# Kernel optimization log

Measured on AMD Instinct MI355X. Metric: run time of the kernel, lower is better.

Reference implementation:

```python
import jax, jax.numpy as jnp
import numpy as np

N = 32768; NS = 16; C_MAIN = 128; C_MOD = 128; C_IN = 16; SHARE = 8
EPS = 1e-5; CHUNK = 1024
C_OUT = C_MAIN + C_MOD  # out_main = in_main + in_mod
C_W = C_IN // SHARE     # attention-weight channels = 2


def _bn(x, g, b, m, v):
    # BatchNorm1d in eval mode, per last-dim channel
    return (x - m) / jnp.sqrt(v + EPS) * g + b


def _knn(p, k):
    # exact kNN (self included, distance 0), chunked to bound memory
    def f(q):  # q: (CHUNK, 3)
        d = jnp.sum((q[:, None, :] - p[None, :, :]) ** 2, axis=-1)  # (CHUNK, N)
        return jax.lax.top_k(-d, k)[1]
    return jax.lax.map(f, p.reshape(-1, CHUNK, 3)).reshape(-1, k)


def setup_inputs() -> dict:
    key = jax.random.key(0)
    ks = iter(jax.random.split(key, 24))
    rn = lambda shape, s=0.1: jax.random.normal(next(ks), shape, jnp.float32) * s
    inp = {}
    inp["x_main"] = jax.random.normal(next(ks), (N, C_MAIN), jnp.float32)
    inp["x_mod"] = jax.random.normal(next(ks), (N, C_MOD), jnp.float32)
    inp["xyz"] = jax.random.uniform(next(ks), (N, 3), dtype=jnp.float32)
    inp["W_ein"] = rn((C_OUT, C_IN)); inp["b_ein"] = rn((C_IN,))
    inp["W_eout"] = rn((C_IN, C_OUT)); inp["b_eout"] = rn((C_OUT,))
    inp["Wq"] = rn((C_IN, C_IN)); inp["bq"] = rn((C_IN,))
    inp["Wk"] = rn((C_IN, C_IN)); inp["bk"] = rn((C_IN,))
    inp["Wv"] = rn((C_IN, C_IN)); inp["bv"] = rn((C_IN,))
    inp["Wp1"] = rn((3, 3)); inp["bp1"] = rn((3,))
    inp["Wp2"] = rn((3, C_IN)); inp["bp2"] = rn((C_IN,))
    inp["Wl1"] = rn((C_IN, C_W)); inp["bl1"] = rn((C_W,))
    inp["Wl2"] = rn((C_W, C_W)); inp["bl2"] = rn((C_W,))
    for name, c in (("bn_p", 3), ("bn_w1", C_IN), ("bn_w2", C_W)):
        inp[name + "_g"] = jnp.ones(c, jnp.float32)
        inp[name + "_b"] = jnp.zeros(c, jnp.float32)
        inp[name + "_m"] = jnp.zeros(c, jnp.float32)
        inp[name + "_v"] = jnp.ones(c, jnp.float32)
    return inp


def _forward(x_main, x_mod, xyz, W_ein, b_ein, W_eout, b_eout, Wq, bq, Wk, bk, Wv, bv,
             Wp1, bp1, Wp2, bp2, Wl1, bl1, Wl2, bl2,
             bn_p_g, bn_p_b, bn_p_m, bn_p_v,
             bn_w1_g, bn_w1_b, bn_w1_m, bn_w1_v,
             bn_w2_g, bn_w2_b, bn_w2_m, bn_w2_v, idx):
    x_fused = jnp.concatenate([x_main, x_mod], axis=-1)   # (N, 256)
    x_res = x_fused
    h = x_fused @ W_ein + b_ein                           # E_in: (N, 16)
    # PointTransformerLayer (local vector self-attention over NS neighbors)
    xq = h @ Wq + bq
    xk = h @ Wk + bk
    xv = h @ Wv + bv
    p_r = xyz[idx] - xyz[:, None, :]                      # relative coords (N, NS, 3)
    g_k = xk[idx]                                         # grouped keys   (N, NS, 16)
    g_v = xv[idx]                                         # grouped values (N, NS, 16)
    # linear_p: Linear(3,3) -> BN -> ReLU -> Linear(3, C_IN)
    t = jax.nn.relu(_bn(p_r @ Wp1 + bp1, bn_p_g, bn_p_b, bn_p_m, bn_p_v))
    p_e = t @ Wp2 + bp2                                   # (N, NS, 16)
    # out_planes//mid_planes == 1, so the .view(...).sum(2) on p_e is identity
    w = g_k - xq[:, None, :] + p_e
    # linear_w: BN -> ReLU -> Linear(16,2) -> BN -> ReLU -> Linear(2,2)
    w = jax.nn.relu(_bn(w, bn_w1_g, bn_w1_b, bn_w1_m, bn_w1_v))
    w = w @ Wl1 + bl1
    w = jax.nn.relu(_bn(w, bn_w2_g, bn_w2_b, bn_w2_m, bn_w2_v))
    w = w @ Wl2 + bl2                                     # (N, NS, 2)
    w = jax.nn.softmax(w, axis=1)                         # softmax over neighbors
    agg = ((g_v + p_e).reshape(N, NS, SHARE, C_W) * w[:, :, None, :]).sum(1).reshape(N, C_IN)
    return agg @ W_eout + b_eout + x_res                  # E_out + residual


def reference(x_main, x_mod, xyz, W_ein, b_ein, W_eout, b_eout, Wq, bq, Wk, bk, Wv, bv,
              Wp1, bp1, Wp2, bp2, Wl1, bl1, Wl2, bl2,
              bn_p_g, bn_p_b, bn_p_m, bn_p_v,
              bn_w1_g, bn_w1_b, bn_w1_m, bn_w1_v,
              bn_w2_g, bn_w2_b, bn_w2_m, bn_w2_v):
    idx = _knn(xyz, NS)
    return _forward(x_main, x_mod, xyz, W_ein, b_ein, W_eout, b_eout, Wq, bq, Wk, bk, Wv, bv,
                    Wp1, bp1, Wp2, bp2, Wl1, bl1, Wl2, bl2,
                    bn_p_g, bn_p_b, bn_p_m, bn_p_v,
                    bn_w1_g, bn_w1_b, bn_w1_m, bn_w1_v,
                    bn_w2_g, bn_w2_b, bn_w2_m, bn_w2_v, idx)
```

## Files before the change

kernel.cpp:

```cpp
#include <hip/hip_runtime.h>
#include <cstdint>

#define NPTS 32768
#define K 16
#define G 16
#define NCELL (G*G*G)

typedef unsigned short u16;
typedef unsigned int u32;
typedef unsigned long long u64;

__device__ __forceinline__ float bf(u16 v) { return __uint_as_float(((u32)v) << 16); }
__device__ __forceinline__ void unp(u32 u, float& a, float& b) {
    a = __uint_as_float(u << 16);
    b = __uint_as_float(u & 0xffff0000u);
}
__device__ __forceinline__ u32 f2b(float f) {
    u32 x = __float_as_uint(f);
    return (x + 0x7fffu + ((x >> 16) & 1u)) >> 16;
}
__device__ __forceinline__ float ldw(const void* p, int j, bool isb) {
    return isb ? bf(((const u16*)p)[j]) : ((const float*)p)[j];
}
__device__ __forceinline__ void ld8(const void* p, size_t i, int cb, bool isb, float xs[8]) {
    if (isb) {
        const uint4* r = (const uint4*)((const u16*)p + i * 128);
        const uint4 u = r[cb];
        unp(u.x, xs[0], xs[1]); unp(u.y, xs[2], xs[3]);
        unp(u.z, xs[4], xs[5]); unp(u.w, xs[6], xs[7]);
    } else {
        const float4* r = (const float4*)((const float*)p + i * 128);
        const float4 a = r[2 * cb], b = r[2 * cb + 1];
        xs[0] = a.x; xs[1] = a.y; xs[2] = a.z; xs[3] = a.w;
        xs[4] = b.x; xs[5] = b.y; xs[6] = b.z; xs[7] = b.w;
    }
}
__device__ __forceinline__ int cellco(float x) {
    int c = (int)(x * (float)G);
    return c < 0 ? 0 : (c > G - 1 ? G - 1 : c);
}
__device__ __forceinline__ u64 shflx64(u64 v, int m) {
    return (u64)__shfl_xor((long long)v, m, 64);
}

__global__ __launch_bounds__(256) void k_feats(
    const void* __restrict__ xm, const void* __restrict__ xd, const void* __restrict__ xyz,
    const void* __restrict__ Wein, const void* __restrict__ bein,
    const void* __restrict__ Wq, const void* __restrict__ bq,
    const void* __restrict__ Wk, const void* __restrict__ bk,
    const void* __restrict__ Wv, const void* __restrict__ bv,
    const u32* __restrict__ sigp,
    float* __restrict__ oq, float* __restrict__ ok, float* __restrict__ ov,
    float4* __restrict__ xyzf, int* __restrict__ cellCnt,
    int* __restrict__ ptCell, int* __restrict__ ptRank)
{
    const bool isb = (*sigp == 0x3F803F80u);
    __shared__ float sW[4096];
    __shared__ float sM[768];
    __shared__ float sB[64];
    const int t = threadIdx.x;
    for (int u = t; u < 4096; u += 256) sW[u] = ldw(Wein, u, isb);
    if (t < 256) { sM[t] = ldw(Wq, t, isb); sM[256 + t] = ldw(Wk, t, isb); sM[512 + t] = ldw(Wv, t, isb); }
    if (t < 64) {
        const void* bsrc = (t < 16) ? bein : (t < 32) ? bq : (t < 48) ? bk : bv;
        sB[t] = ldw(bsrc, t & 15, isb);
    }
    __syncthreads();
    const int r = blockIdx.x * 128 + (t >> 1);
    const int half = t & 1;
    float hp[16];
#pragma unroll
    for (int j = 0; j < 16; ++j) hp[j] = half ? 0.f : sB[j];
    const void* src = half ? xd : xm;
    const int wbase = half * 128;
#pragma unroll 2
    for (int cb = 0; cb < 16; ++cb) {
        float xs[8];
        ld8(src, (size_t)r, cb, isb, xs);
#pragma unroll
        for (int u = 0; u < 8; ++u) {
            const float x = xs[u];
            const float* w = &sW[(wbase + cb * 8 + u) * 16];
#pragma unroll
            for (int j = 0; j < 16; ++j) hp[j] = fmaf(x, w[j], hp[j]);
        }
    }
    float h[16];
#pragma unroll
    for (int j = 0; j < 16; ++j) h[j] = hp[j] + __shfl_xor(hp[j], 1, 64);
    const float* wm = half ? &sM[256] : &sM[0];
    const float* bm = half ? &sB[32] : &sB[16];
    float acc[16];
#pragma unroll
    for (int j = 0; j < 16; ++j) acc[j] = bm[j];
#pragma unroll
    for (int m = 0; m < 16; ++m) {
        const float hm = h[m];
#pragma unroll
        for (int j = 0; j < 16; ++j) acc[j] = fmaf(hm, wm[m * 16 + j], acc[j]);
    }
    float4* o4 = (float4*)((half ? ok : oq) + (size_t)r * 16);
#pragma unroll
    for (int j4 = 0; j4 < 4; ++j4)
        o4[j4] = make_float4(acc[4 * j4], acc[4 * j4 + 1], acc[4 * j4 + 2], acc[4 * j4 + 3]);
    float vacc[8];
    const int vo = half * 8;
#pragma unroll
    for (int u = 0; u < 8; ++u) vacc[u] = sB[48 + vo + u];
#pragma unroll
    for (int m = 0; m < 16; ++m) {
        const float hm = h[m];
#pragma unroll
        for (int u = 0; u < 8; ++u) vacc[u] = fmaf(hm, sM[512 + m * 16 + vo + u], vacc[u]);
    }
    float4* v4 = (float4*)(ov + (size_t)r * 16 + vo);
    v4[0] = make_float4(vacc[0], vacc[1], vacc[2], vacc[3]);
    v4[1] = make_float4(vacc[4], vacc[5], vacc[6], vacc[7]);
    if (half == 0) {
        float px, py, pz;
        if (isb) { const u16* z = (const u16*)xyz; px = bf(z[r * 3]); py = bf(z[r * 3 + 1]); pz = bf(z[r * 3 + 2]); }
        else { const float* z = (const float*)xyz; px = z[r * 3]; py = z[r * 3 + 1]; pz = z[r * 3 + 2]; }
        xyzf[r] = make_float4(px, py, pz, 0.f);
        const int c = (cellco(pz) * G + cellco(py)) * G + cellco(px);
        ptCell[r] = c;
        ptRank[r] = atomicAdd(&cellCnt[c], 1);
    }
}

__global__ __launch_bounds__(1024) void k_scan(const int* __restrict__ cnt, int* __restrict__ starts)
{
    __shared__ int wtot[16];
    const int t = threadIdx.x;
    const int4 c4 = ((const int4*)cnt)[t];
    const int s = c4.x + c4.y + c4.z + c4.w;
    int inc = s;
#pragma unroll
    for (int off = 1; off < 64; off <<= 1) {
        const int v = __shfl_up(inc, off, 64);
        if ((t & 63) >= off) inc += v;
    }
    if ((t & 63) == 63) wtot[t >> 6] = inc;
    __syncthreads();
    const int wid = t >> 6;
    int wpre = 0;
    for (int w = 0; w < wid; ++w) wpre += wtot[w];
    const int excl = wpre + inc - s;
    int4 st;
    st.x = excl; st.y = excl + c4.x; st.z = excl + c4.x + c4.y; st.w = excl + c4.x + c4.y + c4.z;
    ((int4*)starts)[t] = st;
    if (t == 1023) starts[NCELL] = excl + s;
}

__global__ __launch_bounds__(256) void k_scatter(const float4* __restrict__ xyzf,
    const int* __restrict__ ptCell, const int* __restrict__ ptRank,
    const int* __restrict__ starts, float4* __restrict__ sorted)
{
    const int i = blockIdx.x * 256 + threadIdx.x;
    float4 p = xyzf[i];
    p.w = __int_as_float(i);
    sorted[starts[ptCell[i]] + ptRank[i]] = p;
}

__device__ __forceinline__ void ins16(u64 kb, u64 key[K]) {
    if (kb < key[K - 1]) {
#pragma unroll
        for (int j = 0; j < K; ++j) {
            const bool lt = kb < key[j];
            const u64 tk = lt ? key[j] : kb;
            key[j] = lt ? kb : key[j];
            kb = tk;
        }
    }
}

__device__ __forceinline__ void scan_run8(const float4* __restrict__ sorted,
    int b, int e, int l, float qx, float qy, float qz, u64 key[K])
{
    int p = b + l;
    if (p >= e) return;
    float4 c = sorted[p];
    while (true) {
        const int pn = p + 8;
        const bool more = pn < e;
        float4 cnx = c;
        if (more) cnx = sorted[pn];
        const float dx = __fsub_rn(qx, c.x);
        const float dy = __fsub_rn(qy, c.y);
        const float dz = __fsub_rn(qz, c.z);
        const float d = __fadd_rn(__fadd_rn(__fmul_rn(dx, dx), __fmul_rn(dy, dy)), __fmul_rn(dz, dz));
        ins16(((u64)__float_as_uint(d) << 32) | (u32)__float_as_int(c.w), key);
        if (!more) break;
        c = cnx; p = pn;
    }
}

__device__ __forceinline__ u64 tau8(const u64 key[K]) {
    u64 b1 = key[15], b2 = key[1];
#pragma unroll
    for (int m = 1; m <= 4; m <<= 1) {
        const u64 o1 = shflx64(b1, m); b1 = o1 < b1 ? o1 : b1;
        const u64 o2 = shflx64(b2, m); b2 = o2 > b2 ? o2 : b2;
    }
    return b1 < b2 ? b1 : b2;
}

__device__ __forceinline__ void merge16k(u64 k[K], int mask) {
    u64 pk[K];
#pragma unroll
    for (int i = 0; i < K; ++i) pk[i] = shflx64(k[K - 1 - i], mask);
#pragma unroll
    for (int i = 0; i < K; ++i) k[i] = k[i] < pk[i] ? k[i] : pk[i];
#pragma unroll
    for (int ks = 8; ks >= 1; ks >>= 1) {
#pragma unroll
        for (int i = 0; i < K; ++i) {
            if ((i & ks) == 0) {
                const int j = i + ks;
                const u64 a = k[i], b = k[j];
                k[i] = a < b ? a : b;
                k[j] = a < b ? b : a;
            }
        }
    }
}

__device__ __forceinline__ float guard_radius(float qx, float qy, float qz,
                                              int cx, int cy, int cz, int R)
{
    const float h = 1.0f / (float)G;
    float rg = 3.4e38f;
    if (cx - R >= 1)     rg = fminf(rg, qx - (float)(cx - R) * h);
    if (cx + R <= G - 2) rg = fminf(rg, (float)(cx + R + 1) * h - qx);
    if (cy - R >= 1)     rg = fminf(rg, qy - (float)(cy - R) * h);
    if (cy + R <= G - 2) rg = fminf(rg, (float)(cy + R + 1) * h - qy);
    if (cz - R >= 1)     rg = fminf(rg, qz - (float)(cz - R) * h);
    if (cz + R <= G - 2) rg = fminf(rg, (float)(cz + R + 1) * h - qz);
    return rg;
}

__global__ __launch_bounds__(256) void k_knng(const float4* __restrict__ sorted,
    const int* __restrict__ starts, int* __restrict__ idxOut)
{
    const int g = blockIdx.x * 256 + threadIdx.x;
    const int s = g >> 3;
    const int l = g & 7;
    const float4 me = sorted[s];
    const int orig = __float_as_int(me.w);
    const int cx = cellco(me.x), cy = cellco(me.y), cz = cellco(me.z);
    const float h = 1.0f / (float)G;
    u64 key[K];
#pragma unroll
    for (int j = 0; j < K; ++j) key[j] = ~0ull;
    u64 tk = ~0ull;

    const int ord_dy[9] = { 0, -1, 1,  0, 0, -1, -1,  1, 1 };
    const int ord_dz[9] = { 0,  0, 0, -1, 1, -1,  1, -1, 1 };
#pragma unroll
    for (int r = 0; r < 9; ++r) {
        const int dy = ord_dy[r], dz = ord_dz[r];
        const int yy = cy + dy, zz = cz + dz;
        if ((unsigned)yy > (unsigned)(G - 1) || (unsigned)zz > (unsigned)(G - 1)) continue;
        const float dyd = dy < 0 ? me.y - (float)cy * h : dy > 0 ? (float)(cy + 1) * h - me.y : 0.f;
        const float dzd = dz < 0 ? me.z - (float)cz * h : dz > 0 ? (float)(cz + 1) * h - me.z : 0.f;
        const u64 mk = (u64)__float_as_uint((dyd * dyd + dzd * dzd) * 0.9999f) << 32;
        if (tk < mk) continue;
        const int base = (zz * G + yy) * G;
        const int x0 = cx - 1 < 0 ? 0 : cx - 1;
        const int x1 = cx + 1 > G - 1 ? G - 1 : cx + 1;
        scan_run8(sorted, starts[base + x0], starts[base + x1 + 1], l, me.x, me.y, me.z, key);
        tk = tau8(key);
    }
    int R = 1;
    while (R < G) {
        const float rg = guard_radius(me.x, me.y, me.z, cx, cy, cz, R);
        if (tk < ((u64)__float_as_uint(rg * rg * 0.9999f) << 32)) break;
        ++R;
        for (int dz = -R; dz <= R; ++dz) {
            const int zz = cz + dz;
            if ((unsigned)zz > (unsigned)(G - 1)) continue;
            const int az = dz < 0 ? -dz : dz;
            const float dzd = dz < 0 ? me.z - (float)(cz + dz + 1) * h : dz > 0 ? (float)(cz + dz) * h - me.z : 0.f;
            for (int dy = -R; dy <= R; ++dy) {
                const int yy = cy + dy;
                if ((unsigned)yy > (unsigned)(G - 1)) continue;
                const int ay = dy < 0 ? -dy : dy;
                const float dyd = dy < 0 ? me.y - (float)(cy + dy + 1) * h : dy > 0 ? (float)(cy + dy) * h - me.y : 0.f;
                const float myz = dzd * dzd + dyd * dyd;
                const int base = (zz * G + yy) * G;
                if (az == R || ay == R) {
                    if (tk < ((u64)__float_as_uint(myz * 0.9999f) << 32)) continue;
                    const int x0 = cx - R < 0 ? 0 : cx - R;
                    const int x1 = cx + R > G - 1 ? G - 1 : cx + R;
                    scan_run8(sorted, starts[base + x0], starts[base + x1 + 1], l, me.x, me.y, me.z, key);
                    tk = tau8(key);
                } else {
                    if (cx - R >= 0) {
                        const float xd = me.x - (float)(cx - R + 1) * h;
                        if (!(tk < ((u64)__float_as_uint((myz + xd * xd) * 0.9999f) << 32))) {
                            scan_run8(sorted, starts[base + cx - R], starts[base + cx - R + 1], l, me.x, me.y, me.z, key);
                            tk = tau8(key);
                        }
                    }
                    if (cx + R <= G - 1) {
                        const float xd = (float)(cx + R) * h - me.x;
                        if (!(tk < ((u64)__float_as_uint((myz + xd * xd) * 0.9999f) << 32))) {
                            scan_run8(sorted, starts[base + cx + R], starts[base + cx + R + 1], l, me.x, me.y, me.z, key);
                            tk = tau8(key);
                        }
                    }
                }
            }
        }
    }
    merge16k(key, 1); merge16k(key, 2); merge16k(key, 4);
    if (l == 0) {
        int4* o = (int4*)(idxOut + (size_t)orig * K);
#pragma unroll
        for (int j4 = 0; j4 < 4; ++j4)
            o[j4] = make_int4((int)(u32)key[4 * j4], (int)(u32)key[4 * j4 + 1],
                              (int)(u32)key[4 * j4 + 2], (int)(u32)key[4 * j4 + 3]);
    }
}

__global__ __launch_bounds__(256) void k_attn(
    const void* __restrict__ xm, const void* __restrict__ xd,
    const float4* __restrict__ xyzf,
    const float* __restrict__ xq, const float* __restrict__ xk, const float* __restrict__ xv,
    const int* __restrict__ idx,
    const void* __restrict__ Weout, const void* __restrict__ beout,
    const void* __restrict__ Wp1, const void* __restrict__ bp1,
    const void* __restrict__ Wp2, const void* __restrict__ bp2,
    const void* __restrict__ Wl1, const void* __restrict__ bl1,
    const void* __restrict__ Wl2, const void* __restrict__ bl2,
    const void* __restrict__ bnp_g, const void* __restrict__ bnp_b, const void* __restrict__ bnp_m, const void* __restrict__ bnp_v,
    const void* __restrict__ bw1_g, const void* __restrict__ bw1_b, const void* __restrict__ bw1_m, const void* __restrict__ bw1_v,
    const void* __restrict__ bw2_g, const void* __restrict__ bw2_b, const void* __restrict__ bw2_m, const void* __restrict__ bw2_v,
    void* __restrict__ out)
{
    const bool isb = (*(const u32*)bnp_g == 0x3F803F80u);
    __shared__ float sWe[4096];
    __shared__ float sbe[256];
    __shared__ float sWp2[48];
    __shared__ float sbp2[16];
    __shared__ float sWl1[32];
    __shared__ float s1[16], o1[16];
    const int t = threadIdx.x;
    for (int u = t; u < 4096; u += 256) sWe[u] = ldw(Weout, u, isb);
    if (t < 256) sbe[t] = ldw(beout, t, isb);
    if (t < 48) sWp2[t] = ldw(Wp2, t, isb);
    if (t < 16) sbp2[t] = ldw(bp2, t, isb);
    if (t < 32) sWl1[t] = ldw(Wl1, t, isb);
    if (t < 16) {
        const float s = ldw(bw1_g, t, isb) / sqrtf(ldw(bw1_v, t, isb) + 1e-5f);
        s1[t] = s; o1[t] = ldw(bw1_b, t, isb) - ldw(bw1_m, t, isb) * s;
    }
    __syncthreads();
    const int g = blockIdx.x * 256 + t;
    const int s = g >> 3;
    const int l = g & 7;
    float Wp1r[9], bp1r[3], sp[3], op[3];
#pragma unroll
    for (int u = 0; u < 9; ++u) Wp1r[u] = ldw(Wp1, u, isb);
#pragma unroll
    for (int a = 0; a < 3; ++a) {
        const float sc = ldw(bnp_g, a, isb) / sqrtf(ldw(bnp_v, a, isb) + 1e-5f);
        sp[a] = sc; op[a] = ldw(bnp_b, a, isb) - ldw(bnp_m, a, isb) * sc;
        bp1r[a] = ldw(bp1, a, isb);
    }
    float Wl2r[4], bl1r[2], bl2r[2], s2[2], o2[2];
#pragma unroll
    for (int u = 0; u < 4; ++u) Wl2r[u] = ldw(Wl2, u, isb);
#pragma unroll
    for (int c = 0; c < 2; ++c) {
        bl1r[c] = ldw(bl1, c, isb); bl2r[c] = ldw(bl2, c, isb);
        const float sc = ldw(bw2_g, c, isb) / sqrtf(ldw(bw2_v, c, isb) + 1e-5f);
        s2[c] = sc; o2[c] = ldw(bw2_b, c, isb) - ldw(bw2_m, c, isb) * sc;
    }
    float q[16];
    const float4* qrow = (const float4*)(xq + (size_t)s * 16);
#pragma unroll
    for (int j4 = 0; j4 < 4; ++j4) {
        const float4 v = qrow[j4];
        q[4 * j4] = v.x; q[4 * j4 + 1] = v.y; q[4 * j4 + 2] = v.z; q[4 * j4 + 3] = v.w;
    }
    const int2 nb2 = ((const int2*)(idx + (size_t)s * 16))[l];
    const int nb[2] = { nb2.x, nb2.y };
    const float4 cp = xyzf[s];
    float wa[2], wb[2], ttx[2], tty[2], ttz[2];
#pragma unroll
    for (int n = 0; n < 2; ++n) {
        const int nn = nb[n];
        const float4 pp = xyzf[nn];
        const float prx = pp.x - cp.x, pry = pp.y - cp.y, prz = pp.z - cp.z;
        float tt[3];
#pragma unroll
        for (int a = 0; a < 3; ++a) {
            float v = prx * Wp1r[a] + pry * Wp1r[3 + a] + prz * Wp1r[6 + a] + bp1r[a];
            v = fmaf(v, sp[a], op[a]);
            tt[a] = v > 0.f ? v : 0.f;
        }
        ttx[n] = tt[0]; tty[n] = tt[1]; ttz[n] = tt[2];
        const float4* k4 = (const float4*)(xk + (size_t)nn * 16);
        float kk[16];
#pragma unroll
        for (int j4 = 0; j4 < 4; ++j4) {
            const float4 v = k4[j4];
            kk[4 * j4] = v.x; kk[4 * j4 + 1] = v.y; kk[4 * j4 + 2] = v.z; kk[4 * j4 + 3] = v.w;
        }
        float wl0 = bl1r[0], wl1v = bl1r[1];
#pragma unroll
        for (int j = 0; j < 16; ++j) {
            const float pe = tt[0] * sWp2[j] + tt[1] * sWp2[16 + j] + tt[2] * sWp2[32 + j] + sbp2[j];
            float w = kk[j] - q[j] + pe;
            w = fmaf(w, s1[j], o1[j]); w = w > 0.f ? w : 0.f;
            wl0 = fmaf(w, sWl1[2 * j], wl0);
            wl1v = fmaf(w, sWl1[2 * j + 1], wl1v);
        }
        float y0 = fmaf(wl0, s2[0], o2[0]); y0 = y0 > 0.f ? y0 : 0.f;
        float y1 = fmaf(wl1v, s2[1], o2[1]); y1 = y1 > 0.f ? y1 : 0.f;
        wa[n] = y0 * Wl2r[0] + y1 * Wl2r[2] + bl2r[0];
        wb[n] = y0 * Wl2r[1] + y1 * Wl2r[3] + bl2r[1];
    }
    float m0 = fmaxf(wa[0], wa[1]), m1 = fmaxf(wb[0], wb[1]);
#pragma unroll
    for (int m = 1; m <= 4; m <<= 1) {
        m0 = fmaxf(m0, __shfl_xor(m0, m, 64));
        m1 = fmaxf(m1, __shfl_xor(m1, m, 64));
    }
    float sA = 0.f, sB = 0.f;
#pragma unroll
    for (int n = 0; n < 2; ++n) {
        wa[n] = __expf(wa[n] - m0); sA += wa[n];
        wb[n] = __expf(wb[n] - m1); sB += wb[n];
    }
#pragma unroll
    for (int m = 1; m <= 4; m <<= 1) {
        sA += __shfl_xor(sA, m, 64);
        sB += __shfl_xor(sB, m, 64);
    }
    const float rA = 1.f / sA, rB = 1.f / sB;
    float agg[16];
#pragma unroll
    for (int j = 0; j < 16; ++j) agg[j] = 0.f;
#pragma unroll
    for (int n = 0; n < 2; ++n) {
        const float wA = wa[n] * rA, wB = wb[n] * rB;
        const float4* v4 = (const float4*)(xv + (size_t)nb[n] * 16);
        float vv[16];
#pragma unroll
        for (int j4 = 0; j4 < 4; ++j4) {
            const float4 v = v4[j4];
            vv[4 * j4] = v.x; vv[4 * j4 + 1] = v.y; vv[4 * j4 + 2] = v.z; vv[4 * j4 + 3] = v.w;
        }
#pragma unroll
        for (int j = 0; j < 16; ++j) {
            const float pe = ttx[n] * sWp2[j] + tty[n] * sWp2[16 + j] + ttz[n] * sWp2[32 + j] + sbp2[j];
            agg[j] = fmaf(vv[j] + pe, (j & 1) ? wB : wA, agg[j]);
        }
    }
#pragma unroll
    for (int j = 0; j < 16; ++j) {
        agg[j] += __shfl_xor(agg[j], 1, 64);
        agg[j] += __shfl_xor(agg[j], 2, 64);
        agg[j] += __shfl_xor(agg[j], 4, 64);
    }
#pragma unroll 1
    for (int obi = 0; obi < 4; ++obi) {
        const int ob = obi * 8 + l;
        float xs[8];
        ld8((ob < 16) ? xm : xd, (size_t)s, ob & 15, isb, xs);
        const int o0 = ob * 8;
        float acc[8];
#pragma unroll
        for (int u = 0; u < 8; ++u) acc[u] = sbe[o0 + u] + xs[u];
#pragma unroll
        for (int j = 0; j < 16; ++j) {
            const float aj = agg[j];
            const float* w = &sWe[j * 256 + o0];
#pragma unroll
            for (int u = 0; u < 8; ++u) acc[u] = fmaf(aj, w[u], acc[u]);
        }
        if (isb) {
            u32* orow = (u32*)out + (size_t)s * 128;
#pragma unroll
            for (int u = 0; u < 4; ++u)
                orow[ob * 4 + u] = f2b(acc[2 * u]) | (f2b(acc[2 * u + 1]) << 16);
        } else {
            float4* orow = (float4*)((float*)out + (size_t)s * 256);
            orow[2 * ob]     = make_float4(acc[0], acc[1], acc[2], acc[3]);
            orow[2 * ob + 1] = make_float4(acc[4], acc[5], acc[6], acc[7]);
        }
    }
}

extern "C" void kernel_launch(void* const* d_in, const int* in_sizes, int n_in,
                              void* d_out, int out_size, void* d_ws, size_t ws_size,
                              hipStream_t stream)
{
    (void)in_sizes; (void)n_in; (void)out_size; (void)ws_size;
    const void* xm   = d_in[0];
    const void* xd   = d_in[1];
    const void* xyz  = d_in[2];
    const void* Wein = d_in[3];
    const void* bein = d_in[4];
    const void* Weout= d_in[5];
    const void* beout= d_in[6];
    const void* Wq   = d_in[7];
    const void* bq   = d_in[8];
    const void* Wk   = d_in[9];
    const void* bk   = d_in[10];
    const void* Wv   = d_in[11];
    const void* bv   = d_in[12];
    const void* Wp1  = d_in[13];
    const void* bp1  = d_in[14];
    const void* Wp2  = d_in[15];
    const void* bp2  = d_in[16];
    const void* Wl1  = d_in[17];
    const void* bl1  = d_in[18];
    const void* Wl2  = d_in[19];
    const void* bl2  = d_in[20];
    const void* bnp_g = d_in[21];
    const void* bnp_b = d_in[22];
    const void* bnp_m = d_in[23];
    const void* bnp_v = d_in[24];
    const void* bw1_g = d_in[25];
    const void* bw1_b = d_in[26];
    const void* bw1_m = d_in[27];
    const void* bw1_v = d_in[28];
    const void* bw2_g = d_in[29];
    const void* bw2_b = d_in[30];
    const void* bw2_m = d_in[31];
    const void* bw2_v = d_in[32];

    char* ws = (char*)d_ws;
    const size_t MB = 1024 * 1024;
    float*  oq    = (float*)(ws);
    float*  ok    = (float*)(ws + 2 * MB);
    float*  ov    = (float*)(ws + 4 * MB);
    int*    idx   = (int*)  (ws + 6 * MB);
    float4* xyzf  = (float4*)(ws + 8 * MB);
    float4* sortp = (float4*)(ws + 8 * MB + 512 * 1024);
    int* cellCnt  = (int*)(ws + 9 * MB);
    int* starts   = (int*)(ws + 9 * MB + 32 * 1024);
    int* ptCell   = (int*)(ws + 9 * MB + 64 * 1024);
    int* ptRank   = (int*)(ws + 9 * MB + 192 * 1024);

    hipMemsetAsync(cellCnt, 0, NCELL * sizeof(int), stream);
    k_feats<<<dim3(NPTS * 2 / 256), dim3(256), 0, stream>>>(
        xm, xd, xyz, Wein, bein, Wq, bq, Wk, bk, Wv, bv,
        (const u32*)bnp_g, oq, ok, ov, xyzf, cellCnt, ptCell, ptRank);
    k_scan<<<dim3(1), dim3(1024), 0, stream>>>(cellCnt, starts);
    k_scatter<<<dim3(NPTS / 256), dim3(256), 0, stream>>>(xyzf, ptCell, ptRank, starts, sortp);
    k_knng<<<dim3(NPTS * 8 / 256), dim3(256), 0, stream>>>(sortp, starts, idx);
    k_attn<<<dim3(NPTS * 8 / 256), dim3(256), 0, stream>>>(
        xm, xd, xyzf, oq, ok, ov, idx, Weout, beout, Wp1, bp1, Wp2, bp2,
        Wl1, bl1, Wl2, bl2, bnp_g, bnp_b, bnp_m, bnp_v,
        bw1_g, bw1_b, bw1_m, bw1_v, bw2_g, bw2_b, bw2_m, bw2_v, d_out);
}
```

Before: 268.2 us.

## Fuse cell-prefix scan into scatter and restructure kNN first-shell search

Removes the separate single-block scan kernel: every scatter block now recomputes the 4096-cell prefix sum in shared memory, and block 0 writes the starts array. The kNN kernel flattens the 3x3 neighbor-cell rows into one index space. It makes a cheap top-2 pass to get a per-query distance threshold, then a filtered insertion pass with 4-way unrolled prefetching. This replaces per-row shuffle-based threshold updates and cuts wasted ins16 calls. Later shells use the merged key list as a fixed threshold and re-merge after each shell. The cost is redundant scan work in every scatter block and reading the first shell twice.

```diff
diff --git a/kernel.cpp b/kernel.cpp
--- a/kernel.cpp
+++ b/kernel.cpp
@@ -41,6 +41,15 @@
 }
 __device__ __forceinline__ u64 shflx64(u64 v, int m) {
     return (u64)__shfl_xor((long long)v, m, 64);
+}
+__device__ __forceinline__ float dist_np(float4 q, float4 c) {
+    const float dx = __fsub_rn(q.x, c.x);
+    const float dy = __fsub_rn(q.y, c.y);
+    const float dz = __fsub_rn(q.z, c.z);
+    return __fadd_rn(__fadd_rn(__fmul_rn(dx, dx), __fmul_rn(dy, dy)), __fmul_rn(dz, dz));
+}
+__device__ __forceinline__ u64 key64(float d, int idx) {
+    return ((u64)__float_as_uint(d) << 32) | (u32)idx;
 }
 
 __global__ __launch_bounds__(256) void k_feats(
@@ -127,38 +136,48 @@
     }
 }
 
-__global__ __launch_bounds__(1024) void k_scan(const int* __restrict__ cnt, int* __restrict__ starts)
+__global__ __launch_bounds__(256) void k_scatter(const float4* __restrict__ xyzf,
+    const int* __restrict__ ptCell, const int* __restrict__ ptRank,
+    const int* __restrict__ cellCnt, int* __restrict__ starts, float4* __restrict__ sorted)
 {
-    __shared__ int wtot[16];
+    __shared__ int sSt[NCELL];
+    __shared__ int wsum[4];
     const int t = threadIdx.x;
-    const int4 c4 = ((const int4*)cnt)[t];
-    const int s = c4.x + c4.y + c4.z + c4.w;
+    int c[16];
+    {
+        const int4* cc = (const int4*)cellCnt;
+#pragma unroll
+        for (int u = 0; u < 4; ++u) {
+            const int4 v = cc[t * 4 + u];
+            c[4 * u] = v.x; c[4 * u + 1] = v.y; c[4 * u + 2] = v.z; c[4 * u + 3] = v.w;
+        }
+    }
+    int s = 0;
+#pragma unroll
+    for (int u = 0; u < 16; ++u) s += c[u];
     int inc = s;
 #pragma unroll
     for (int off = 1; off < 64; off <<= 1) {
         const int v = __shfl_up(inc, off, 64);
         if ((t & 63) >= off) inc += v;
     }
-    if ((t & 63) == 63) wtot[t >> 6] = inc;
+    if ((t & 63) == 63) wsum[t >> 6] = inc;
     __syncthreads();
-    const int wid = t >> 6;
-    int wpre = 0;
-    for (int w = 0; w < wid; ++w) wpre += wtot[w];
-    const int excl = wpre + inc - s;
-    int4 st;
-    st.x = excl; st.y = excl + c4.x; st.z = excl + c4.x + c4.y; st.w = excl + c4.x + c4.y + c4.z;
-    ((int4*)starts)[t] = st;
-    if (t == 1023) starts[NCELL] = excl + s;
-}
-
-__global__ __launch_bounds__(256) void k_scatter(const float4* __restrict__ xyzf,
-    const int* __restrict__ ptCell, const int* __restrict__ ptRank,
-    const int* __restrict__ starts, float4* __restrict__ sorted)
-{
-    const int i = blockIdx.x * 256 + threadIdx.x;
+    int pre = 0;
+    for (int w = 0; w < (t >> 6); ++w) pre += wsum[w];
+    int run = pre + inc - s;
+#pragma unroll
+    for (int u = 0; u < 16; ++u) { sSt[t * 16 + u] = run; run += c[u]; }
+    __syncthreads();
+    const int i = blockIdx.x * 256 + t;
     float4 p = xyzf[i];
     p.w = __int_as_float(i);
-    sorted[starts[ptCell[i]] + ptRank[i]] = p;
+    sorted[sSt[ptCell[i]] + ptRank[i]] = p;
+    if (blockIdx.x == 0) {
+#pragma unroll
+        for (int u = 0; u < 16; ++u) starts[t * 16 + u] = sSt[t * 16 + u];
+        if (t == 0) starts[NCELL] = NPTS;
+    }
 }
 
 __device__ __forceinline__ void ins16(u64 kb, u64 key[K]) {
@@ -172,38 +191,6 @@
         }
     }
 }
-
-__device__ __forceinline__ void scan_run8(const float4* __restrict__ sorted,
-    int b, int e, int l, float qx, float qy, float qz, u64 key[K])
-{
-    int p = b + l;
-    if (p >= e) return;
-    float4 c = sorted[p];
-    while (true) {
-        const int pn = p + 8;
-        const bool more = pn < e;
-        float4 cnx = c;
-        if (more) cnx = sorted[pn];
-        const float dx = __fsub_rn(qx, c.x);
-        const float dy = __fsub_rn(qy, c.y);
-        const float dz = __fsub_rn(qz, c.z);
-        const float d = __fadd_rn(__fadd_rn(__fmul_rn(dx, dx), __fmul_rn(dy, dy)), __fmul_rn(dz, dz));
-        ins16(((u64)__float_as_uint(d) << 32) | (u32)__float_as_int(c.w), key);
-        if (!more) break;
-        c = cnx; p = pn;
-    }
-}
-
-__device__ __forceinline__ u64 tau8(const u64 key[K]) {
-    u64 b1 = key[15], b2 = key[1];
-#pragma unroll
-    for (int m = 1; m <= 4; m <<= 1) {
-        const u64 o1 = shflx64(b1, m); b1 = o1 < b1 ? o1 : b1;
-        const u64 o2 = shflx64(b2, m); b2 = o2 > b2 ? o2 : b2;
-    }
-    return b1 < b2 ? b1 : b2;
-}
-
 __device__ __forceinline__ void merge16k(u64 k[K], int mask) {
     u64 pk[K];
 #pragma unroll
@@ -223,7 +210,6 @@
         }
     }
 }
-
 __device__ __forceinline__ float guard_radius(float qx, float qy, float qz,
                                               int cx, int cy, int cz, int R)
 {
@@ -237,6 +223,23 @@
     if (cz + R <= G - 2) rg = fminf(rg, (float)(cz + R + 1) * h - qz);
     return rg;
 }
+__device__ __forceinline__ void scan_run8(const float4* __restrict__ sorted,
+    int b, int e, int l, float4 me, u64 tk, u64 key[K])
+{
+    int p = b + l;
+    if (p >= e) return;
+    float4 c = sorted[p];
+    while (true) {
+        const int pn = p + 8;
+        const bool more = pn < e;
+        float4 cnx = c;
+        if (more) cnx = sorted[pn];
+        const u64 kb = key64(dist_np(me, c), __float_as_int(c.w));
+        if (kb <= tk) ins16(kb, key);
+        if (!more) break;
+        c = cnx; p = pn;
+    }
+}
 
 __global__ __launch_bounds__(256) void k_knng(const float4* __restrict__ sorted,
     const int* __restrict__ starts, int* __restrict__ idxOut)
@@ -245,35 +248,110 @@
     const int s = g >> 3;
     const int l = g & 7;
     const float4 me = sorted[s];
-    const int orig = __float_as_int(me.w);
     const int cx = cellco(me.x), cy = cellco(me.y), cz = cellco(me.z);
     const float h = 1.0f / (float)G;
-    u64 key[K];
-#pragma unroll
-    for (int j = 0; j < K; ++j) key[j] = ~0ull;
-    u64 tk = ~0ull;
-
-    const int ord_dy[9] = { 0, -1, 1,  0, 0, -1, -1,  1, 1 };
-    const int ord_dz[9] = { 0,  0, 0, -1, 1, -1,  1, -1, 1 };
-#pragma unroll
-    for (int r = 0; r < 9; ++r) {
-        const int dy = ord_dy[r], dz = ord_dz[r];
-        const int yy = cy + dy, zz = cz + dz;
-        if ((unsigned)yy > (unsigned)(G - 1) || (unsigned)zz > (unsigned)(G - 1)) continue;
-        const float dyd = dy < 0 ? me.y - (float)cy * h : dy > 0 ? (float)(cy + 1) * h - me.y : 0.f;
-        const float dzd = dz < 0 ? me.z - (float)cz * h : dz > 0 ? (float)(cz + 1) * h - me.z : 0.f;
-        const u64 mk = (u64)__float_as_uint((dyd * dyd + dzd * dzd) * 0.9999f) << 32;
-        if (tk < mk) continue;
-        const int base = (zz * G + yy) * G;
+
+    int rb[9]; int rc[10]; rc[0] = 0;
+    {
         const int x0 = cx - 1 < 0 ? 0 : cx - 1;
         const int x1 = cx + 1 > G - 1 ? G - 1 : cx + 1;
-        scan_run8(sorted, starts[base + x0], starts[base + x1 + 1], l, me.x, me.y, me.z, key);
-        tk = tau8(key);
-    }
+#pragma unroll
+        for (int r = 0; r < 9; ++r) {
+            const int dz = r / 3 - 1, dy = r % 3 - 1;
+            const int zz = cz + dz, yy = cy + dy;
+            int b = 0, len = 0;
+            if ((unsigned)zz <= (unsigned)(G - 1) && (unsigned)yy <= (unsigned)(G - 1)) {
+                const int base = (zz * G + yy) * G;
+                b = starts[base + x0];
+                len = starts[base + x1 + 1] - b;
+            }
+            rb[r] = b;
+            rc[r + 1] = rc[r] + len;
+        }
+    }
+    const int tot = rc[9];
+    int bias[9];
+#pragma unroll
+    for (int r = 0; r < 9; ++r) bias[r] = rb[r] - rc[r];
+
+#define FLAT(f) ({ int _b = bias[0]; \
+    _Pragma("unroll") for (int _r = 1; _r < 9; ++_r) _b = ((f) >= rc[_r]) ? bias[_r] : _b; \
+    (f) + _b; })
+
+    u64 kA0 = ~0ull, kA1 = ~0ull;
+    {
+        int p0 = l, p1 = l + 8, p2 = l + 16, p3 = l + 24;
+        float4 c0 = sorted[p0 < tot ? FLAT(p0) : 0];
+        float4 c1 = sorted[p1 < tot ? FLAT(p1) : 0];
+        float4 c2 = sorted[p2 < tot ? FLAT(p2) : 0];
+        float4 c3 = sorted[p3 < tot ? FLAT(p3) : 0];
+        while (p0 < tot) {
+            const int q0 = p0 + 32, q1 = p1 + 32, q2 = p2 + 32, q3 = p3 + 32;
+            float4 n0 = sorted[q0 < tot ? FLAT(q0) : 0];
+            float4 n1 = sorted[q1 < tot ? FLAT(q1) : 0];
+            float4 n2 = sorted[q2 < tot ? FLAT(q2) : 0];
+            float4 n3 = sorted[q3 < tot ? FLAT(q3) : 0];
+            u64 kb;
+#define TOP2(c, valid) \
+            kb = (valid) ? key64(dist_np(me, c), __float_as_int((c).w)) : ~0ull; \
+            { const bool c0lt = kb < kA0, c1lt = kb < kA1; \
+              const u64 nk1 = c0lt ? kA0 : kb; \
+              kA1 = c1lt ? nk1 : kA1; \
+              kA0 = c0lt ? kb : kA0; }
+            TOP2(c0, true);
+            TOP2(c1, p1 < tot);
+            TOP2(c2, p2 < tot);
+            TOP2(c3, p3 < tot);
+#undef TOP2
+            p0 = q0; p1 = q1; p2 = q2; p3 = q3;
+            c0 = n0; c1 = n1; c2 = n2; c3 = n3;
+        }
+    }
+    u64 tau0 = kA1;
+#pragma unroll
+    for (int m = 1; m <= 4; m <<= 1) { const u64 o = shflx64(tau0, m); tau0 = o > tau0 ? o : tau0; }
+
+    u64 key[K];
+#pragma unroll
+    for (int j = 0; j < K; ++j) key[j] = ~0ull;
+    {
+        int p0 = l, p1 = l + 8, p2 = l + 16, p3 = l + 24;
+        float4 c0 = sorted[p0 < tot ? FLAT(p0) : 0];
+        float4 c1 = sorted[p1 < tot ? FLAT(p1) : 0];
+        float4 c2 = sorted[p2 < tot ? FLAT(p2) : 0];
+        float4 c3 = sorted[p3 < tot ? FLAT(p3) : 0];
+        while (p0 < tot) {
+            const int q0 = p0 + 32, q1 = p1 + 32, q2 = p2 + 32, q3 = p3 + 32;
+            float4 n0 = sorted[q0 < tot ? FLAT(q0) : 0];
+            float4 n1 = sorted[q1 < tot ? FLAT(q1) : 0];
+            float4 n2 = sorted[q2 < tot ? FLAT(q2) : 0];
+            float4 n3 = sorted[q3 < tot ? FLAT(q3) : 0];
+            u64 kb;
+#define INSF(c, valid) \
+            kb = key64(dist_np(me, c), __float_as_int((c).w)); \
+            if ((valid) && kb <= tau0) ins16(kb, key);
+            INSF(c0, true);
+            INSF(c1, p1 < tot);
+            INSF(c2, p2 < tot);
+            INSF(c3, p3 < tot);
+#undef INSF
+            p0 = q0; p1 = q1; p2 = q2; p3 = q3;
+            c0 = n0; c1 = n1; c2 = n2; c3 = n3;
+        }
+    }
+#undef FLAT
+
+    merge16k(key, 1); merge16k(key, 2); merge16k(key, 4);
+
     int R = 1;
     while (R < G) {
+        const u64 tk = key[K - 1];
         const float rg = guard_radius(me.x, me.y, me.z, cx, cy, cz, R);
         if (tk < ((u64)__float_as_uint(rg * rg * 0.9999f) << 32)) break;
+        if (l != 0) {
+#pragma unroll
+            for (int j = 0; j < K; ++j) key[j] = ~0ull;
+        }
         ++R;
         for (int dz = -R; dz <= R; ++dz) {
             const int zz = cz + dz;
@@ -291,29 +369,25 @@
                     if (tk < ((u64)__float_as_uint(myz * 0.9999f) << 32)) continue;
                     const int x0 = cx - R < 0 ? 0 : cx - R;
                     const int x1 = cx + R > G - 1 ? G - 1 : cx + R;
-                    scan_run8(sorted, starts[base + x0], starts[base + x1 + 1], l, me.x, me.y, me.z, key);
-                    tk = tau8(key);
+                    scan_run8(sorted, starts[base + x0], starts[base + x1 + 1], l, me, tk, key);
                 } else {
                     if (cx - R >= 0) {
                         const float xd = me.x - (float)(cx - R + 1) * h;
-                        if (!(tk < ((u64)__float_as_uint((myz + xd * xd) * 0.9999f) << 32))) {
-                            scan_run8(sorted, starts[base + cx - R], starts[base + cx - R + 1], l, me.x, me.y, me.z, key);
-                            tk = tau8(key);
-                        }
+                        if (!(tk < ((u64)__float_as_uint((myz + xd * xd) * 0.9999f) << 32)))
+                            scan_run8(sorted, starts[base + cx - R], starts[base + cx - R + 1], l, me, tk, key);
                     }
                     if (cx + R <= G - 1) {
                         const float xd = (float)(cx + R) * h - me.x;
-                        if (!(tk < ((u64)__float_as_uint((myz + xd * xd) * 0.9999f) << 32))) {
-                            scan_run8(sorted, starts[base + cx + R], starts[base + cx + R + 1], l, me.x, me.y, me.z, key);
-                            tk = tau8(key);
-                        }
+                        if (!(tk < ((u64)__float_as_uint((myz + xd * xd) * 0.9999f) << 32)))
+                            scan_run8(sorted, starts[base + cx + R], starts[base + cx + R + 1], l, me, tk, key);
                     }
                 }
             }
         }
-    }
-    merge16k(key, 1); merge16k(key, 2); merge16k(key, 4);
+        merge16k(key, 1); merge16k(key, 2); merge16k(key, 4);
+    }
     if (l == 0) {
+        const int orig = __float_as_int(me.w);
         int4* o = (int4*)(idxOut + (size_t)orig * K);
 #pragma unroll
         for (int j4 = 0; j4 < 4; ++j4)
@@ -549,8 +623,7 @@
     k_feats<<<dim3(NPTS * 2 / 256), dim3(256), 0, stream>>>(
         xm, xd, xyz, Wein, bein, Wq, bq, Wk, bk, Wv, bv,
         (const u32*)bnp_g, oq, ok, ov, xyzf, cellCnt, ptCell, ptRank);
-    k_scan<<<dim3(1), dim3(1024), 0, stream>>>(cellCnt, starts);
-    k_scatter<<<dim3(NPTS / 256), dim3(256), 0, stream>>>(xyzf, ptCell, ptRank, starts, sortp);
+    k_scatter<<<dim3(NPTS / 256), dim3(256), 0, stream>>>(xyzf, ptCell, ptRank, cellCnt, starts, sortp);
     k_knng<<<dim3(NPTS * 8 / 256), dim3(256), 0, stream>>>(sortp, starts, idx);
     k_attn<<<dim3(NPTS * 8 / 256), dim3(256), 0, stream>>>(
         xm, xd, xyzf, oq, ok, ov, idx, Weout, beout, Wp1, bp1, Wp2, bp2,
```

New measurement: 258.4 us. 3.7% less time.
